# Kernel tuning notes

Measured on AMD Instinct MI355X. Metric: run time of the kernel, lower is better.

Reference implementation:

```python
import jax, jax.numpy as jnp
import numpy as np

N_NODES = 200000
D_FEAT = 128
B = 40000
DEG = 16
E = B * DEG
D_OUT = 256
N_CLASSES = 128


def setup_inputs() -> dict:
    key = jax.random.key(0)
    ks = jax.random.split(key, 8)
    inputs = jax.random.randint(ks[0], (B,), 0, N_NODES)
    neighbor_ids = jax.random.randint(ks[1], (E,), 0, N_NODES)
    segment_ids = jnp.repeat(jnp.arange(B, dtype=jnp.int64 if jax.config.jax_enable_x64 else jnp.int32), DEG)
    feat_data = jax.random.normal(ks[2], (N_NODES, D_FEAT), dtype=jnp.float32)
    W1 = jax.random.normal(ks[3], (D_OUT, 2 * D_FEAT), dtype=jnp.float32) * 0.05
    b1 = jax.random.normal(ks[4], (D_OUT,), dtype=jnp.float32) * 0.05
    W3 = jax.random.normal(ks[5], (N_CLASSES, D_OUT), dtype=jnp.float32) * 0.05
    b3 = jax.random.normal(ks[6], (N_CLASSES,), dtype=jnp.float32) * 0.05
    return {"inputs": inputs, "neighbor_ids": neighbor_ids, "segment_ids": segment_ids,
            "feat_data": feat_data, "W1": W1, "b1": b1, "W3": W3, "b3": b3}


def reference(inputs, neighbor_ids, segment_ids, feat_data, W1, b1, W3, b3):
    # Segment-mean over neighbor features (replaces Python per-node loop)
    neigh = feat_data[neighbor_ids]                               # [E, D]
    sums = jax.ops.segment_sum(neigh, segment_ids, num_segments=B)  # [B, D]
    cnt = jax.ops.segment_sum(jnp.ones((E,), jnp.float32), segment_ids, num_segments=B)
    means = sums / jnp.maximum(cnt, 1.0)[:, None]                 # [B, D]
    # Concat self + neighbor-mean, linear1
    emb = jnp.concatenate([feat_data[inputs], means], axis=1)     # [B, 2D]
    h = emb @ W1.T + b1                                           # [B, D_OUT]
    # ReLU -> linear3 -> L2 normalize (F.normalize, eps=1e-12)
    logits = jax.nn.relu(h) @ W3.T + b3                           # [B, n_classes]
    norm = jnp.linalg.norm(logits, axis=1, keepdims=True)
    return logits / jnp.maximum(norm, 1e-12)
```

## Files before the change

### kernel.cpp

```cpp
#include <hip/hip_runtime.h>
#include <stdint.h>

#define NNODES 200000
#define BNODES 40000
#define DEG    16
#define DFEAT  128
#define DOUT   256
#define NCLS   128
#define TILE   32

typedef __attribute__((ext_vector_type(8))) __bf16 bf16x8;
typedef __attribute__((ext_vector_type(4))) float  floatx4;

__device__ __forceinline__ uint32_t f2bf(float f) {
  uint32_t x = __float_as_uint(f);
  return ((x + 0x7fffu + ((x >> 16) & 1u)) >> 16) & 0xffffu;
}

__global__ void cvt_weights(const float* __restrict__ W1, const float* __restrict__ W3,
                            uint16_t* __restrict__ w1b, uint16_t* __restrict__ w3b) {
  int i = blockIdx.x * 256 + threadIdx.x;
  if (i < DOUT * 2 * DFEAT) w1b[i] = (uint16_t)f2bf(W1[i]);
  if (i < NCLS * DOUT)      w3b[i] = (uint16_t)f2bf(W3[i]);
}

__global__ __launch_bounds__(256) void sage_fused(
    const int* __restrict__ inputs, const int* __restrict__ nbr,
    const float* __restrict__ feat,
    const uint16_t* __restrict__ w1b, const float* __restrict__ b1,
    const uint16_t* __restrict__ w3b, const float* __restrict__ b3,
    float* __restrict__ out) {
  __shared__ __align__(16) uint16_t embL[TILE][264];
  __shared__ __align__(16) uint16_t hL[TILE][264];
  __shared__ __align__(16) float    lgL[TILE][132];

  const int tid  = threadIdx.x;
  const int w    = tid >> 6;
  const int lane = tid & 63;
  const int quad = lane >> 4;
  const int l16  = lane & 15;

  {
    const int nodeBase = blockIdx.x * TILE + w * 8;
#pragma unroll
    for (int n = 0; n < 8; ++n) {
      const int node = nodeBase + n;
      const int row  = w * 8 + n;
      const int* nb  = nbr + node * DEG;
      float sx = 0.f, sy = 0.f;
#pragma unroll
      for (int j = 0; j < DEG; ++j) {
        const float2 v = *(const float2*)(feat + (size_t)nb[j] * DFEAT + lane * 2);
        sx += v.x; sy += v.y;
      }
      const float2 sv = *(const float2*)(feat + (size_t)inputs[node] * DFEAT + lane * 2);
      const uint32_t selfp = f2bf(sv.x) | (f2bf(sv.y) << 16);
      const uint32_t meanp = f2bf(sx * 0.0625f) | (f2bf(sy * 0.0625f) << 16);
      *(uint32_t*)&embL[row][lane * 2]         = selfp;
      *(uint32_t*)&embL[row][DFEAT + lane * 2] = meanp;
    }
  }
  __syncthreads();

  const int kq = quad * 8;

  {
    floatx4 acc[2][4];
#pragma unroll
    for (int mt = 0; mt < 2; ++mt)
#pragma unroll
      for (int ot = 0; ot < 4; ++ot) {
        floatx4 z = {0.f, 0.f, 0.f, 0.f};
        acc[mt][ot] = z;
      }
#pragma unroll
    for (int kt = 0; kt < 8; ++kt) {
      const int k0 = kt * 32 + kq;
      const bf16x8 a0 = *(const bf16x8*)&embL[l16][k0];
      const bf16x8 a1 = *(const bf16x8*)&embL[16 + l16][k0];
#pragma unroll
      for (int ot = 0; ot < 4; ++ot) {
        const int o = (w * 4 + ot) * 16 + l16;
        const bf16x8 b = *(const bf16x8*)(w1b + o * 256 + k0);
        acc[0][ot] = __builtin_amdgcn_mfma_f32_16x16x32_bf16(a0, b, acc[0][ot], 0, 0, 0);
        acc[1][ot] = __builtin_amdgcn_mfma_f32_16x16x32_bf16(a1, b, acc[1][ot], 0, 0, 0);
      }
    }
#pragma unroll
    for (int ot = 0; ot < 4; ++ot) {
      const int o = (w * 4 + ot) * 16 + l16;
      const float bias = b1[o];
#pragma unroll
      for (int mt = 0; mt < 2; ++mt)
#pragma unroll
        for (int r = 0; r < 4; ++r) {
          float v = acc[mt][ot][r] + bias;
          v = fmaxf(v, 0.f);
          hL[mt * 16 + quad * 4 + r][o] = (uint16_t)f2bf(v);
        }
    }
  }
  __syncthreads();

  {
    floatx4 acc2[2][2];
#pragma unroll
    for (int mt = 0; mt < 2; ++mt)
#pragma unroll
      for (int ct = 0; ct < 2; ++ct) {
        floatx4 z = {0.f, 0.f, 0.f, 0.f};
        acc2[mt][ct] = z;
      }
#pragma unroll
    for (int kt = 0; kt < 8; ++kt) {
      const int k0 = kt * 32 + kq;
      const bf16x8 a0 = *(const bf16x8*)&hL[l16][k0];
      const bf16x8 a1 = *(const bf16x8*)&hL[16 + l16][k0];
#pragma unroll
      for (int ct = 0; ct < 2; ++ct) {
        const int c = (w * 2 + ct) * 16 + l16;
        const bf16x8 b = *(const bf16x8*)(w3b + c * 256 + k0);
        acc2[0][ct] = __builtin_amdgcn_mfma_f32_16x16x32_bf16(a0, b, acc2[0][ct], 0, 0, 0);
        acc2[1][ct] = __builtin_amdgcn_mfma_f32_16x16x32_bf16(a1, b, acc2[1][ct], 0, 0, 0);
      }
    }
#pragma unroll
    for (int ct = 0; ct < 2; ++ct) {
      const int c = (w * 2 + ct) * 16 + l16;
      const float bias = b3[c];
#pragma unroll
      for (int mt = 0; mt < 2; ++mt)
#pragma unroll
        for (int r = 0; r < 4; ++r)
          lgL[mt * 16 + quad * 4 + r][c] = acc2[mt][ct][r] + bias;
    }
  }
  __syncthreads();

  {
    const int nr  = tid >> 3;
    const int sub = tid & 7;
    const float* lrow = &lgL[nr][sub * 16];
    float4 v0 = *(const float4*)(lrow + 0);
    float4 v1 = *(const float4*)(lrow + 4);
    float4 v2 = *(const float4*)(lrow + 8);
    float4 v3 = *(const float4*)(lrow + 12);
    float ss = v0.x * v0.x + v0.y * v0.y + v0.z * v0.z + v0.w * v0.w
             + v1.x * v1.x + v1.y * v1.y + v1.z * v1.z + v1.w * v1.w
             + v2.x * v2.x + v2.y * v2.y + v2.z * v2.z + v2.w * v2.w
             + v3.x * v3.x + v3.y * v3.y + v3.z * v3.z + v3.w * v3.w;
    ss += __shfl_xor(ss, 1);
    ss += __shfl_xor(ss, 2);
    ss += __shfl_xor(ss, 4);
    const float scale = 1.f / fmaxf(sqrtf(ss), 1e-12f);
    v0.x *= scale; v0.y *= scale; v0.z *= scale; v0.w *= scale;
    v1.x *= scale; v1.y *= scale; v1.z *= scale; v1.w *= scale;
    v2.x *= scale; v2.y *= scale; v2.z *= scale; v2.w *= scale;
    v3.x *= scale; v3.y *= scale; v3.z *= scale; v3.w *= scale;
    float* op = out + ((size_t)(blockIdx.x * TILE + nr)) * NCLS + sub * 16;
    *(float4*)(op + 0)  = v0;
    *(float4*)(op + 4)  = v1;
    *(float4*)(op + 8)  = v2;
    *(float4*)(op + 12) = v3;
  }
}

extern "C" void kernel_launch(void* const* d_in, const int* in_sizes, int n_in,
                              void* d_out, int out_size, void* d_ws, size_t ws_size,
                              hipStream_t stream) {
  const int*   inputs = (const int*)d_in[0];
  const int*   nbr    = (const int*)d_in[1];
  const float* feat   = (const float*)d_in[3];
  const float* W1     = (const float*)d_in[4];
  const float* b1     = (const float*)d_in[5];
  const float* W3     = (const float*)d_in[6];
  const float* b3     = (const float*)d_in[7];

  uint16_t* w1b = (uint16_t*)d_ws;
  uint16_t* w3b = w1b + DOUT * 2 * DFEAT;

  cvt_weights<<<(DOUT * 2 * DFEAT) / 256, 256, 0, stream>>>(W1, W3, w1b, w3b);
  sage_fused<<<BNODES / TILE, 256, 0, stream>>>(inputs, nbr, feat, w1b, b1, w3b, b3,
                                                (float*)d_out);
}
```

Baseline: 218.0 us.

## Batch neighbor gathers two nodes at a time and alias shared buffers

Restructures the neighbor-mean gather so each wave issues all 34 feature-row loads for two nodes before reducing, increasing memory-level parallelism. The reduction becomes a tree sum, slightly changing float rounding. The embedding and logits shared buffers are aliased to reduce LDS footprint, and launch bounds request 4 blocks per SIMD to raise occupancy. This risks register pressure from holding 32 float2 values per lane.

New measurement: 215.9 us. No clear change (-0.9%).

```diff
diff --git a/kernel.cpp b/kernel.cpp
--- a/kernel.cpp
+++ b/kernel.cpp
@@ -17,47 +17,67 @@
   return ((x + 0x7fffu + ((x >> 16) & 1u)) >> 16) & 0xffffu;
 }
 
-__global__ void cvt_weights(const float* __restrict__ W1, const float* __restrict__ W3,
-                            uint16_t* __restrict__ w1b, uint16_t* __restrict__ w3b) {
+__global__ __launch_bounds__(256) void cvt_weights(
+    const float* __restrict__ W1, const float* __restrict__ W3,
+    uint16_t* __restrict__ w1b, uint16_t* __restrict__ w3b) {
   int i = blockIdx.x * 256 + threadIdx.x;
   if (i < DOUT * 2 * DFEAT) w1b[i] = (uint16_t)f2bf(W1[i]);
   if (i < NCLS * DOUT)      w3b[i] = (uint16_t)f2bf(W3[i]);
 }
 
-__global__ __launch_bounds__(256) void sage_fused(
+__global__ __launch_bounds__(256, 4) void sage_fused(
     const int* __restrict__ inputs, const int* __restrict__ nbr,
     const float* __restrict__ feat,
     const uint16_t* __restrict__ w1b, const float* __restrict__ b1,
     const uint16_t* __restrict__ w3b, const float* __restrict__ b3,
     float* __restrict__ out) {
-  __shared__ __align__(16) uint16_t embL[TILE][264];
+  __shared__ __align__(16) unsigned char smemA[TILE * 264 * 2];
   __shared__ __align__(16) uint16_t hL[TILE][264];
-  __shared__ __align__(16) float    lgL[TILE][132];
+  uint16_t (*embL)[264] = (uint16_t (*)[264])smemA;
+  float    (*lgL)[132]  = (float    (*)[132])smemA;
 
   const int tid  = threadIdx.x;
-  const int w    = tid >> 6;
+  const int w    = __builtin_amdgcn_readfirstlane(tid >> 6);
   const int lane = tid & 63;
   const int quad = lane >> 4;
   const int l16  = lane & 15;
 
   {
     const int nodeBase = blockIdx.x * TILE + w * 8;
-#pragma unroll
-    for (int n = 0; n < 8; ++n) {
-      const int node = nodeBase + n;
-      const int row  = w * 8 + n;
-      const int* nb  = nbr + node * DEG;
-      float sx = 0.f, sy = 0.f;
-#pragma unroll
-      for (int j = 0; j < DEG; ++j) {
-        const float2 v = *(const float2*)(feat + (size_t)nb[j] * DFEAT + lane * 2);
-        sx += v.x; sy += v.y;
-      }
-      const float2 sv = *(const float2*)(feat + (size_t)inputs[node] * DFEAT + lane * 2);
-      const uint32_t selfp = f2bf(sv.x) | (f2bf(sv.y) << 16);
-      const uint32_t meanp = f2bf(sx * 0.0625f) | (f2bf(sy * 0.0625f) << 16);
-      *(uint32_t*)&embL[row][lane * 2]         = selfp;
-      *(uint32_t*)&embL[row][DFEAT + lane * 2] = meanp;
+    const float* fb = feat + lane * 2;
+#pragma unroll
+    for (int pp = 0; pp < 8; pp += 2) {
+      const int nA = nodeBase + pp, nB = nodeBase + pp + 1;
+      const int* nbA = nbr + nA * DEG;
+      const int* nbB = nbr + nB * DEG;
+      const int sA = inputs[nA], sB = inputs[nB];
+      float2 rA[16], rB[16];
+#pragma unroll
+      for (int j = 0; j < 16; ++j)
+        rA[j] = *(const float2*)(fb + (size_t)nbA[j] * DFEAT);
+      const float2 svA = *(const float2*)(fb + (size_t)sA * DFEAT);
+#pragma unroll
+      for (int j = 0; j < 16; ++j)
+        rB[j] = *(const float2*)(fb + (size_t)nbB[j] * DFEAT);
+      const float2 svB = *(const float2*)(fb + (size_t)sB * DFEAT);
+      {
+        const float sx = (((rA[0].x + rA[1].x) + (rA[2].x + rA[3].x)) + ((rA[4].x + rA[5].x) + (rA[6].x + rA[7].x)))
+                       + (((rA[8].x + rA[9].x) + (rA[10].x + rA[11].x)) + ((rA[12].x + rA[13].x) + (rA[14].x + rA[15].x)));
+        const float sy = (((rA[0].y + rA[1].y) + (rA[2].y + rA[3].y)) + ((rA[4].y + rA[5].y) + (rA[6].y + rA[7].y)))
+                       + (((rA[8].y + rA[9].y) + (rA[10].y + rA[11].y)) + ((rA[12].y + rA[13].y) + (rA[14].y + rA[15].y)));
+        const int row = w * 8 + pp;
+        *(uint32_t*)&embL[row][lane * 2]         = f2bf(svA.x) | (f2bf(svA.y) << 16);
+        *(uint32_t*)&embL[row][DFEAT + lane * 2] = f2bf(sx * 0.0625f) | (f2bf(sy * 0.0625f) << 16);
+      }
+      {
+        const float sx = (((rB[0].x + rB[1].x) + (rB[2].x + rB[3].x)) + ((rB[4].x + rB[5].x) + (rB[6].x + rB[7].x)))
+                       + (((rB[8].x + rB[9].x) + (rB[10].x + rB[11].x)) + ((rB[12].x + rB[13].x) + (rB[14].x + rB[15].x)));
+        const float sy = (((rB[0].y + rB[1].y) + (rB[2].y + rB[3].y)) + ((rB[4].y + rB[5].y) + (rB[6].y + rB[7].y)))
+                       + (((rB[8].y + rB[9].y) + (rB[10].y + rB[11].y)) + ((rB[12].y + rB[13].y) + (rB[14].y + rB[15].y)));
+        const int row = w * 8 + pp + 1;
+        *(uint32_t*)&embL[row][lane * 2]         = f2bf(svB.x) | (f2bf(svB.y) << 16);
+        *(uint32_t*)&embL[row][DFEAT + lane * 2] = f2bf(sx * 0.0625f) | (f2bf(sy * 0.0625f) << 16);
+      }
     }
   }
   __syncthreads();
@@ -180,6 +200,6 @@
   uint16_t* w3b = w1b + DOUT * 2 * DFEAT;
 
   cvt_weights<<<(DOUT * 2 * DFEAT) / 256, 256, 0, stream>>>(W1, W3, w1b, w3b);
-  sage_fused<<<BNODES / TILE, 256, 0, stream>>>(inputs, nbr, feat, w1b, b1, w3b, b3,
-                                                (float*)d_out);
-}
+  sage_fused<<<BNODES / TILE, 256, 0, stream>>>(inputs, nbr, feat, w1b, b1,
+                                                w3b, b3, (float*)d_out);
+}
```
